# Kernel optimization log

Measured on AMD Instinct MI355X. Metric: run time of the kernel, lower is better.

## Reference

```python
import jax, jax.numpy as jnp
import numpy as np


def setup_inputs() -> dict:
    key = jax.random.key(0)
    k1, k2 = jax.random.split(key)
    inputs = jax.random.normal(k1, (4, 8, 24, 24, 64), dtype=jnp.float32)
    gamma = jax.random.normal(k2, (1,), dtype=jnp.float32)
    return {"inputs": inputs, "gamma": gamma}


def reference(inputs, gamma):
    # inputs: (B, D, H, W, C); flatten spatial dims to N = D*H*W
    B, D, H, W, C = inputs.shape
    N = D * H * W
    q = inputs.reshape(B, N, C)                       # proj_query (B, N, C)
    # energy = Q @ Q^T -> (B, N, N)
    energy = jnp.einsum('bnc,bmc->bnm', q, q)
    attention = jax.nn.softmax(energy, axis=-1)       # softmax over last axis
    out = jnp.einsum('bnm,bmc->bnc', attention, q)    # (B, N, C)
    out = out.reshape(B, D, H, W, C)
    return gamma * out + inputs
```

## Files before the change

kernel.cpp:

```cpp
#include <hip/hip_runtime.h>

typedef __bf16 bf16_t;
typedef bf16_t bf16x8 __attribute__((ext_vector_type(8)));
typedef float  f32x4  __attribute__((ext_vector_type(4)));
typedef unsigned int u32;
typedef u32    u32x4  __attribute__((ext_vector_type(4)));
typedef unsigned short u16;

#define B_SZ   4
#define N_SZ   4608
#define C_SZ   64
#define KVB    32
#define QROWS  32
#define NKVT   (N_SZ / KVB)
#define NQT    (N_SZ / QROWS)
#define WV     4
#define SPLIT  4
#define TPC    (NKVT / SPLIT)
#define TPW    (TPC / WV)
#define NBLK   (B_SZ * NQT * SPLIT)
#define RSC    1.2011224087864498f
#define THR    11.0f

__device__ __forceinline__ f32x4 mfma16(bf16x8 a, bf16x8 b, f32x4 c) {
  return __builtin_amdgcn_mfma_f32_16x16x32_bf16(a, b, c, 0, 0, 0);
}

__device__ __forceinline__ u32 pk2(float a, float b) {
  u16 ua = __builtin_bit_cast(u16, (bf16_t)a);
  u16 ub = __builtin_bit_cast(u16, (bf16_t)b);
  return (u32)ua | ((u32)ub << 16);
}

__global__ __launch_bounds__(256) void transform_k(
    const float* __restrict__ in, bf16_t* __restrict__ khi,
    bf16_t* __restrict__ klo, bf16_t* __restrict__ vt) {
  __shared__ float tile[64 * 65];
  const int bid = blockIdx.x;
  const int b  = bid / 72;
  const int n0 = (bid - b * 72) * 64;
  const int t  = threadIdx.x;
  {
    const int nl = t >> 2, c0 = (t & 3) * 16;
    const float* src = in + ((size_t)(b * N_SZ + n0 + nl)) * C_SZ + c0;
    float v[16];
    *(float4*)(v +  0) = *(const float4*)(src +  0);
    *(float4*)(v +  4) = *(const float4*)(src +  4);
    *(float4*)(v +  8) = *(const float4*)(src +  8);
    *(float4*)(v + 12) = *(const float4*)(src + 12);
    bf16x8 h8[2], l8[2];
#pragma unroll
    for (int i = 0; i < 16; ++i) {
      const float vs = RSC * v[i];
      bf16_t h = (bf16_t)vs;
      h8[i >> 3][i & 7] = h;
      l8[i >> 3][i & 7] = (bf16_t)(vs - (float)h);
      tile[nl * 65 + c0 + i] = v[i];
    }
    bf16_t* dh = khi + ((size_t)(b * N_SZ + n0 + nl)) * C_SZ + c0;
    bf16_t* dl = klo + ((size_t)(b * N_SZ + n0 + nl)) * C_SZ + c0;
    *(bf16x8*)(dh) = h8[0]; *(bf16x8*)(dh + 8) = h8[1];
    *(bf16x8*)(dl) = l8[0]; *(bf16x8*)(dl + 8) = l8[1];
  }
  __syncthreads();
  {
    const int c = t >> 2, m0 = (t & 3) * 16;
    bf16x8 o[2];
#pragma unroll
    for (int i = 0; i < 16; ++i)
      o[i >> 3][i & 7] = (bf16_t)tile[(m0 + i) * 65 + c];
    bf16_t* dst = vt + ((size_t)(b * C_SZ + c)) * N_SZ + n0 + m0;
    *(bf16x8*)(dst) = o[0]; *(bf16x8*)(dst + 8) = o[1];
  }
}

#define LOAD_TILE(KV0, KH, KL, VF)                                             \
  {                                                                            \
    _Pragma("unroll")                                                          \
    for (int ct = 0; ct < 2; ++ct)                                             \
      _Pragma("unroll")                                                        \
      for (int ks = 0; ks < 2; ++ks) {                                         \
        const size_t a = (size_t)((KV0) + ct * 16 + c15) * C_SZ + ks * 32 + g * 8; \
        KH[ct][ks] = *(const bf16x8*)(kh_b + a);                               \
        KL[ct][ks] = *(const bf16x8*)(kl_b + a);                               \
      }                                                                        \
    _Pragma("unroll")                                                          \
    for (int co = 0; co < 4; ++co)                                             \
      VF[co] = *(const bf16x8*)(vt_b + (size_t)(co * 16 + c15) * N_SZ + (KV0) + g * 8); \
  }

__global__ __launch_bounds__(256, 2) void attn_part(
    const bf16_t* __restrict__ khi, const bf16_t* __restrict__ klo,
    const bf16_t* __restrict__ vt, float* __restrict__ wsO,
    float* __restrict__ wsML) {
  __shared__ float obuf[256 * 36];
  __shared__ float mlbuf[4 * 2 * 2 * 16];

  const int bid0 = blockIdx.x;
  const int g8   = (bid0 & 7) * (NBLK / 8) + (bid0 >> 3);
  const int b    = g8 / (NQT * SPLIT);
  const int rem  = g8 - b * (NQT * SPLIT);
  const int s    = rem / NQT;
  const int qt   = rem - s * NQT;
  const int blk  = (b * NQT + qt) * SPLIT + s;
  const int t  = threadIdx.x;
  const int w  = t >> 6, l = t & 63;
  const int c15 = l & 15, g = l >> 4;

  const bf16_t* kh_b = khi + (size_t)b * N_SZ * C_SZ;
  const bf16_t* kl_b = klo + (size_t)b * N_SZ * C_SZ;
  const bf16_t* vt_b = vt  + (size_t)b * C_SZ * N_SZ;

  bf16x8 qh[2][2], ql[2][2];
#pragma unroll
  for (int j = 0; j < 2; ++j)
#pragma unroll
    for (int ks = 0; ks < 2; ++ks) {
      const size_t a = (size_t)(qt * QROWS + j * 16 + c15) * C_SZ + ks * 32 + g * 8;
      qh[j][ks] = *(const bf16x8*)(kh_b + a);
      ql[j][ks] = *(const bf16x8*)(kl_b + a);
    }

  f32x4 acc[4][2];
#pragma unroll
  for (int co = 0; co < 4; ++co)
#pragma unroll
    for (int j = 0; j < 2; ++j)
      acc[co][j] = (f32x4){0.f, 0.f, 0.f, 0.f};
  float m_j[2] = {-3.0e38f, -3.0e38f}, l_j[2] = {0.f, 0.f};

  const int sA = ((l >> 4) & 1) * 32 + c15;
  const int sB = sA + 16;
  const bool hi_half = (l >= 32);

  bf16x8 khf[2][2], klf[2][2], vf[4];
  LOAD_TILE((s * TPC + w) * KVB, khf, klf, vf);

  for (int it = 0; it < TPW; ++it) {
    const int itn = (it + 1 < TPW) ? it + 1 : 0;
    const int kvn = (s * TPC + w + itn * WV) * KVB;
    bf16x8 nkh[2][2], nkl[2][2], nvf[4];
    LOAD_TILE(kvn, nkh, nkl, nvf);

    f32x4 sv[2][2];
#pragma unroll
    for (int j = 0; j < 2; ++j)
#pragma unroll
      for (int ct = 0; ct < 2; ++ct) {
        f32x4 a = (f32x4){0.f, 0.f, 0.f, 0.f};
#pragma unroll
        for (int ks = 0; ks < 2; ++ks) {
          a = mfma16(khf[ct][ks], qh[j][ks], a);
          a = mfma16(khf[ct][ks], ql[j][ks], a);
          a = mfma16(klf[ct][ks], qh[j][ks], a);
        }
        sv[j][ct] = a;
      }

#pragma unroll
    for (int j = 0; j < 2; ++j) {
      float mx = fmaxf(fmaxf(fmaxf(sv[j][0][0], sv[j][0][1]), fmaxf(sv[j][0][2], sv[j][0][3])),
                       fmaxf(fmaxf(sv[j][1][0], sv[j][1][1]), fmaxf(sv[j][1][2], sv[j][1][3])));
      mx = fmaxf(mx, __shfl_xor(mx, 16, 64));
      mx = fmaxf(mx, __shfl_xor(mx, 32, 64));
      if (__any(mx > m_j[j] + THR)) {
        const float mn = fmaxf(m_j[j], mx);
        const float sc = exp2f(m_j[j] - mn);
        m_j[j] = mn;
        l_j[j] *= sc;
#pragma unroll
        for (int co = 0; co < 4; ++co)
          acc[co][j] *= sc;
      }
      float rs = 0.f;
#pragma unroll
      for (int ct = 0; ct < 2; ++ct)
#pragma unroll
        for (int r = 0; r < 4; ++r) {
          const float e = exp2f(sv[j][ct][r] - m_j[j]);
          sv[j][ct][r] = e;
          rs += e;
        }
      rs += __shfl_xor(rs, 16, 64);
      rs += __shfl_xor(rs, 32, 64);
      l_j[j] += rs;

      const u32 L0 = pk2(sv[j][0][0], sv[j][0][1]);
      const u32 H0 = pk2(sv[j][0][2], sv[j][0][3]);
      const u32 L1 = pk2(sv[j][1][0], sv[j][1][1]);
      const u32 H1 = pk2(sv[j][1][2], sv[j][1][3]);
      const u32 aL0 = (u32)__shfl((int)L0, sA, 64);
      const u32 aL1 = (u32)__shfl((int)L1, sA, 64);
      const u32 aH0 = (u32)__shfl((int)H0, sA, 64);
      const u32 aH1 = (u32)__shfl((int)H1, sA, 64);
      const u32 bL0 = (u32)__shfl((int)L0, sB, 64);
      const u32 bL1 = (u32)__shfl((int)L1, sB, 64);
      const u32 bH0 = (u32)__shfl((int)H0, sB, 64);
      const u32 bH1 = (u32)__shfl((int)H1, sB, 64);
      const u32x4 pw = (u32x4){hi_half ? aL1 : aL0,
                               hi_half ? aH1 : aH0,
                               hi_half ? bL1 : bL0,
                               hi_half ? bH1 : bH0};
      const bf16x8 pfv = __builtin_bit_cast(bf16x8, pw);
#pragma unroll
      for (int co = 0; co < 4; ++co)
        acc[co][j] = mfma16(vf[co], pfv, acc[co][j]);
    }

#pragma unroll
    for (int ct = 0; ct < 2; ++ct)
#pragma unroll
      for (int ks = 0; ks < 2; ++ks) {
        khf[ct][ks] = nkh[ct][ks];
        klf[ct][ks] = nkl[ct][ks];
      }
#pragma unroll
    for (int co = 0; co < 4; ++co)
      vf[co] = nvf[co];
  }

  float* ob = obuf + (size_t)(w * 64 + l) * 36;
#pragma unroll
  for (int co = 0; co < 4; ++co)
#pragma unroll
    for (int j = 0; j < 2; ++j)
      *(f32x4*)(ob + (co * 2 + j) * 4) = acc[co][j];
  if (g == 0) {
#pragma unroll
    for (int j = 0; j < 2; ++j) {
      mlbuf[((w * 2 + j) * 2 + 0) * 16 + c15] = m_j[j];
      mlbuf[((w * 2 + j) * 2 + 1) * 16 + c15] = l_j[j];
    }
  }
  __syncthreads();

  float* pO  = wsO  + (size_t)blk * (QROWS * C_SZ);
  float* pML = wsML + (size_t)blk * (QROWS * 2);
#pragma unroll
  for (int j = 0; j < 2; ++j) {
    float mw[4];
#pragma unroll
    for (int wp = 0; wp < 4; ++wp)
      mw[wp] = mlbuf[((wp * 2 + j) * 2 + 0) * 16 + c15];
    const float ms = fmaxf(fmaxf(mw[0], mw[1]), fmaxf(mw[2], mw[3]));
    float ls = 0.f;
    f32x4 mg = (f32x4){0.f, 0.f, 0.f, 0.f};
#pragma unroll
    for (int wp = 0; wp < 4; ++wp) {
      const float cf = exp2f(mw[wp] - ms);
      ls += cf * mlbuf[((wp * 2 + j) * 2 + 1) * 16 + c15];
      const f32x4 pv = *(const f32x4*)(obuf + (size_t)(wp * 64 + l) * 36 + (w * 2 + j) * 4);
      mg += pv * cf;
    }
    const int q  = j * 16 + c15;
    const int cb = w * 16 + g * 4;
    *(f32x4*)&pO[q * C_SZ + cb] = mg;
    if (w == 0 && g == 0) {
      pML[q * 2 + 0] = ms;
      pML[q * 2 + 1] = ls;
    }
  }
}

__global__ __launch_bounds__(256) void combine_k(
    const float* __restrict__ in, const float* __restrict__ gamma_p,
    const float* __restrict__ wsO, const float* __restrict__ wsML,
    float* __restrict__ out) {
  const int bid = blockIdx.x;
  const int b   = bid / NQT;
  const int qt  = bid - b * NQT;
  const int t   = threadIdx.x;
  const int q   = t >> 3;
  const int c0  = (t & 7) * 8;
  const int blk0 = bid * SPLIT;

  float m[SPLIT], lv[SPLIT];
  f32x4 o0[SPLIT], o1[SPLIT];
#pragma unroll
  for (int s = 0; s < SPLIT; ++s) {
    const float* pML = wsML + (size_t)(blk0 + s) * (QROWS * 2);
    m[s]  = pML[q * 2 + 0];
    lv[s] = pML[q * 2 + 1];
    const float* pO = wsO + (size_t)(blk0 + s) * (QROWS * C_SZ) + q * C_SZ + c0;
    o0[s] = *(const f32x4*)(pO);
    o1[s] = *(const f32x4*)(pO + 4);
  }
  const float ms = fmaxf(fmaxf(m[0], m[1]), fmaxf(m[2], m[3]));
  float ls = 0.f;
  f32x4 a0 = (f32x4){0.f, 0.f, 0.f, 0.f};
  f32x4 a1 = (f32x4){0.f, 0.f, 0.f, 0.f};
#pragma unroll
  for (int s = 0; s < SPLIT; ++s) {
    const float cf = exp2f(m[s] - ms);
    ls += cf * lv[s];
    a0 += o0[s] * cf;
    a1 += o1[s] * cf;
  }
  const float sc = gamma_p[0] / ls;
  const int row = qt * QROWS + q;
  const size_t base = ((size_t)(b * N_SZ + row)) * C_SZ + c0;
  const float4 i0 = *(const float4*)(in + base);
  const float4 i1 = *(const float4*)(in + base + 4);
  float4 v0, v1;
  v0.x = a0[0] * sc + i0.x; v0.y = a0[1] * sc + i0.y;
  v0.z = a0[2] * sc + i0.z; v0.w = a0[3] * sc + i0.w;
  v1.x = a1[0] * sc + i1.x; v1.y = a1[1] * sc + i1.y;
  v1.z = a1[2] * sc + i1.z; v1.w = a1[3] * sc + i1.w;
  *(float4*)(out + base)     = v0;
  *(float4*)(out + base + 4) = v1;
}

extern "C" void kernel_launch(void* const* d_in, const int* in_sizes, int n_in,
                              void* d_out, int out_size, void* d_ws, size_t ws_size,
                              hipStream_t stream) {
  const float* in = (const float*)d_in[0];
  const float* gp = (const float*)d_in[1];
  float* op = (float*)d_out;
  const size_t plane = (size_t)B_SZ * N_SZ * C_SZ;
  bf16_t* khi = (bf16_t*)d_ws;
  bf16_t* klo = khi + plane;
  bf16_t* vt  = klo + plane;
  float*  wsO  = (float*)((char*)d_ws + 3 * plane * sizeof(bf16_t));
  float*  wsML = wsO + (size_t)NBLK * (QROWS * C_SZ);

  hipLaunchKernelGGL(transform_k, dim3(288), dim3(256), 0, stream, in, khi, klo, vt);
  hipLaunchKernelGGL(attn_part, dim3(NBLK), dim3(256), 0, stream,
                     khi, klo, vt, wsO, wsML);
  hipLaunchKernelGGL(combine_k, dim3(B_SZ * NQT), dim3(256), 0, stream,
                     in, gp, wsO, wsML, op);
}
```

Before: 187.8 us.

## Switch attention inner loop to 32x32x16 MFMA with permlane32 swap for P

Reworks the split-KV attention kernel to use 32x32x16 bf16 MFMA tiles instead of 16x16x32. Each wave now computes a full 32x32 score tile, and the probability fragment is rearranged with permlane32_swap rather than eight cross-lane shuffles. The exp uses raw v_exp_f32, and the occupancy hint is raised from 2 to 4 blocks per CU. The explicit register double-buffered prefetch of K/V tiles is dropped, which may expose load latency; the higher occupancy is meant to hide it instead.

```diff
diff --git a/kernel.cpp b/kernel.cpp
--- a/kernel.cpp
+++ b/kernel.cpp
@@ -3,8 +3,10 @@
 typedef __bf16 bf16_t;
 typedef bf16_t bf16x8 __attribute__((ext_vector_type(8)));
 typedef float  f32x4  __attribute__((ext_vector_type(4)));
+typedef float  f32x16 __attribute__((ext_vector_type(16)));
 typedef unsigned int u32;
 typedef u32    u32x4  __attribute__((ext_vector_type(4)));
+typedef int    i32x2  __attribute__((ext_vector_type(2)));
 typedef unsigned short u16;
 
 #define B_SZ   4
@@ -22,14 +24,22 @@
 #define RSC    1.2011224087864498f
 #define THR    11.0f
 
-__device__ __forceinline__ f32x4 mfma16(bf16x8 a, bf16x8 b, f32x4 c) {
-  return __builtin_amdgcn_mfma_f32_16x16x32_bf16(a, b, c, 0, 0, 0);
-}
-
+__device__ __forceinline__ f32x16 mfma32(bf16x8 a, bf16x8 b, f32x16 c) {
+  return __builtin_amdgcn_mfma_f32_32x32x16_bf16(a, b, c, 0, 0, 0);
+}
 __device__ __forceinline__ u32 pk2(float a, float b) {
   u16 ua = __builtin_bit_cast(u16, (bf16_t)a);
   u16 ub = __builtin_bit_cast(u16, (bf16_t)b);
   return (u32)ua | ((u32)ub << 16);
+}
+__device__ __forceinline__ float ex2(float x) {
+  float r;
+  asm("v_exp_f32 %0, %1" : "=v"(r) : "v"(x));
+  return r;
+}
+__device__ __forceinline__ void plswap(u32& a, u32& b) {
+  i32x2 r = __builtin_amdgcn_permlane32_swap((int)a, (int)b, false, false);
+  a = (u32)r.x; b = (u32)r.y;
 }
 
 __global__ __launch_bounds__(256) void transform_k(
@@ -74,27 +84,12 @@
   }
 }
 
-#define LOAD_TILE(KV0, KH, KL, VF)                                             \
-  {                                                                            \
-    _Pragma("unroll")                                                          \
-    for (int ct = 0; ct < 2; ++ct)                                             \
-      _Pragma("unroll")                                                        \
-      for (int ks = 0; ks < 2; ++ks) {                                         \
-        const size_t a = (size_t)((KV0) + ct * 16 + c15) * C_SZ + ks * 32 + g * 8; \
-        KH[ct][ks] = *(const bf16x8*)(kh_b + a);                               \
-        KL[ct][ks] = *(const bf16x8*)(kl_b + a);                               \
-      }                                                                        \
-    _Pragma("unroll")                                                          \
-    for (int co = 0; co < 4; ++co)                                             \
-      VF[co] = *(const bf16x8*)(vt_b + (size_t)(co * 16 + c15) * N_SZ + (KV0) + g * 8); \
-  }
-
-__global__ __launch_bounds__(256, 2) void attn_part(
+__global__ __launch_bounds__(256, 4) void attn_part(
     const bf16_t* __restrict__ khi, const bf16_t* __restrict__ klo,
     const bf16_t* __restrict__ vt, float* __restrict__ wsO,
     float* __restrict__ wsML) {
-  __shared__ float obuf[256 * 36];
-  __shared__ float mlbuf[4 * 2 * 2 * 16];
+  __shared__ float obuf[256 * 33];
+  __shared__ float mlbuf[WV][2][32];
 
   const int bid0 = blockIdx.x;
   const int g8   = (bid0 & 7) * (NBLK / 8) + (bid0 >> 3);
@@ -105,159 +100,133 @@
   const int blk  = (b * NQT + qt) * SPLIT + s;
   const int t  = threadIdx.x;
   const int w  = t >> 6, l = t & 63;
-  const int c15 = l & 15, g = l >> 4;
+  const int q31 = l & 31, h = l >> 5;
 
   const bf16_t* kh_b = khi + (size_t)b * N_SZ * C_SZ;
   const bf16_t* kl_b = klo + (size_t)b * N_SZ * C_SZ;
   const bf16_t* vt_b = vt  + (size_t)b * C_SZ * N_SZ;
 
-  bf16x8 qh[2][2], ql[2][2];
-#pragma unroll
-  for (int j = 0; j < 2; ++j)
-#pragma unroll
-    for (int ks = 0; ks < 2; ++ks) {
-      const size_t a = (size_t)(qt * QROWS + j * 16 + c15) * C_SZ + ks * 32 + g * 8;
-      qh[j][ks] = *(const bf16x8*)(kh_b + a);
-      ql[j][ks] = *(const bf16x8*)(kl_b + a);
-    }
-
-  f32x4 acc[4][2];
-#pragma unroll
-  for (int co = 0; co < 4; ++co)
-#pragma unroll
-    for (int j = 0; j < 2; ++j)
-      acc[co][j] = (f32x4){0.f, 0.f, 0.f, 0.f};
-  float m_j[2] = {-3.0e38f, -3.0e38f}, l_j[2] = {0.f, 0.f};
-
-  const int sA = ((l >> 4) & 1) * 32 + c15;
-  const int sB = sA + 16;
-  const bool hi_half = (l >= 32);
-
-  bf16x8 khf[2][2], klf[2][2], vf[4];
-  LOAD_TILE((s * TPC + w) * KVB, khf, klf, vf);
+  bf16x8 qh[4], ql[4];
+  {
+    const bf16_t* qrh = kh_b + (size_t)(qt * QROWS + q31) * C_SZ + 8 * h;
+    const bf16_t* qrl = kl_b + (size_t)(qt * QROWS + q31) * C_SZ + 8 * h;
+#pragma unroll
+    for (int ks = 0; ks < 4; ++ks) {
+      qh[ks] = *(const bf16x8*)(qrh + 16 * ks);
+      ql[ks] = *(const bf16x8*)(qrl + 16 * ks);
+    }
+  }
+
+  f32x16 acc0 = {0,0,0,0,0,0,0,0,0,0,0,0,0,0,0,0};
+  f32x16 acc1 = {0,0,0,0,0,0,0,0,0,0,0,0,0,0,0,0};
+  float m_r = -3.0e38f, l_r = 0.f;
 
   for (int it = 0; it < TPW; ++it) {
-    const int itn = (it + 1 < TPW) ? it + 1 : 0;
-    const int kvn = (s * TPC + w + itn * WV) * KVB;
-    bf16x8 nkh[2][2], nkl[2][2], nvf[4];
-    LOAD_TILE(kvn, nkh, nkl, nvf);
-
-    f32x4 sv[2][2];
-#pragma unroll
-    for (int j = 0; j < 2; ++j)
-#pragma unroll
-      for (int ct = 0; ct < 2; ++ct) {
-        f32x4 a = (f32x4){0.f, 0.f, 0.f, 0.f};
-#pragma unroll
-        for (int ks = 0; ks < 2; ++ks) {
-          a = mfma16(khf[ct][ks], qh[j][ks], a);
-          a = mfma16(khf[ct][ks], ql[j][ks], a);
-          a = mfma16(klf[ct][ks], qh[j][ks], a);
-        }
-        sv[j][ct] = a;
+    const int kv0 = (s * TPC + w + it * WV) * KVB;
+
+    bf16x8 kah[4], kal[4];
+    {
+      const bf16_t* krh = kh_b + (size_t)(kv0 + q31) * C_SZ + 8 * h;
+      const bf16_t* krl = kl_b + (size_t)(kv0 + q31) * C_SZ + 8 * h;
+#pragma unroll
+      for (int ks = 0; ks < 4; ++ks) {
+        kah[ks] = *(const bf16x8*)(krh + 16 * ks);
+        kal[ks] = *(const bf16x8*)(krl + 16 * ks);
       }
-
-#pragma unroll
-    for (int j = 0; j < 2; ++j) {
-      float mx = fmaxf(fmaxf(fmaxf(sv[j][0][0], sv[j][0][1]), fmaxf(sv[j][0][2], sv[j][0][3])),
-                       fmaxf(fmaxf(sv[j][1][0], sv[j][1][1]), fmaxf(sv[j][1][2], sv[j][1][3])));
-      mx = fmaxf(mx, __shfl_xor(mx, 16, 64));
-      mx = fmaxf(mx, __shfl_xor(mx, 32, 64));
-      if (__any(mx > m_j[j] + THR)) {
-        const float mn = fmaxf(m_j[j], mx);
-        const float sc = exp2f(m_j[j] - mn);
-        m_j[j] = mn;
-        l_j[j] *= sc;
-#pragma unroll
-        for (int co = 0; co < 4; ++co)
-          acc[co][j] *= sc;
-      }
-      float rs = 0.f;
-#pragma unroll
-      for (int ct = 0; ct < 2; ++ct)
-#pragma unroll
-        for (int r = 0; r < 4; ++r) {
-          const float e = exp2f(sv[j][ct][r] - m_j[j]);
-          sv[j][ct][r] = e;
-          rs += e;
-        }
-      rs += __shfl_xor(rs, 16, 64);
-      rs += __shfl_xor(rs, 32, 64);
-      l_j[j] += rs;
-
-      const u32 L0 = pk2(sv[j][0][0], sv[j][0][1]);
-      const u32 H0 = pk2(sv[j][0][2], sv[j][0][3]);
-      const u32 L1 = pk2(sv[j][1][0], sv[j][1][1]);
-      const u32 H1 = pk2(sv[j][1][2], sv[j][1][3]);
-      const u32 aL0 = (u32)__shfl((int)L0, sA, 64);
-      const u32 aL1 = (u32)__shfl((int)L1, sA, 64);
-      const u32 aH0 = (u32)__shfl((int)H0, sA, 64);
-      const u32 aH1 = (u32)__shfl((int)H1, sA, 64);
-      const u32 bL0 = (u32)__shfl((int)L0, sB, 64);
-      const u32 bL1 = (u32)__shfl((int)L1, sB, 64);
-      const u32 bH0 = (u32)__shfl((int)H0, sB, 64);
-      const u32 bH1 = (u32)__shfl((int)H1, sB, 64);
-      const u32x4 pw = (u32x4){hi_half ? aL1 : aL0,
-                               hi_half ? aH1 : aH0,
-                               hi_half ? bL1 : bL0,
-                               hi_half ? bH1 : bH0};
-      const bf16x8 pfv = __builtin_bit_cast(bf16x8, pw);
-#pragma unroll
-      for (int co = 0; co < 4; ++co)
-        acc[co][j] = mfma16(vf[co], pfv, acc[co][j]);
-    }
-
-#pragma unroll
-    for (int ct = 0; ct < 2; ++ct)
-#pragma unroll
-      for (int ks = 0; ks < 2; ++ks) {
-        khf[ct][ks] = nkh[ct][ks];
-        klf[ct][ks] = nkl[ct][ks];
-      }
-#pragma unroll
-    for (int co = 0; co < 4; ++co)
-      vf[co] = nvf[co];
-  }
-
-  float* ob = obuf + (size_t)(w * 64 + l) * 36;
-#pragma unroll
-  for (int co = 0; co < 4; ++co)
-#pragma unroll
-    for (int j = 0; j < 2; ++j)
-      *(f32x4*)(ob + (co * 2 + j) * 4) = acc[co][j];
-  if (g == 0) {
-#pragma unroll
-    for (int j = 0; j < 2; ++j) {
-      mlbuf[((w * 2 + j) * 2 + 0) * 16 + c15] = m_j[j];
-      mlbuf[((w * 2 + j) * 2 + 1) * 16 + c15] = l_j[j];
-    }
+    }
+
+    f32x16 sv = {0,0,0,0,0,0,0,0,0,0,0,0,0,0,0,0};
+#pragma unroll
+    for (int ks = 0; ks < 4; ++ks) {
+      sv = mfma32(kah[ks], qh[ks], sv);
+      sv = mfma32(kah[ks], ql[ks], sv);
+      sv = mfma32(kal[ks], qh[ks], sv);
+    }
+
+    bf16x8 va[2][2];
+#pragma unroll
+    for (int cb = 0; cb < 2; ++cb)
+#pragma unroll
+      for (int ki = 0; ki < 2; ++ki)
+        va[cb][ki] = *(const bf16x8*)(vt_b + (size_t)(cb * 32 + q31) * N_SZ
+                                      + kv0 + 16 * ki + 8 * h);
+
+    float mx = sv[0];
+#pragma unroll
+    for (int r = 1; r < 16; ++r) mx = fmaxf(mx, sv[r]);
+    mx = fmaxf(mx, __shfl_xor(mx, 32, 64));
+    if (__any(mx > m_r + THR)) {
+      const float mn = fmaxf(m_r, mx);
+      const float sc = ex2(m_r - mn);
+      m_r = mn;
+      l_r *= sc;
+#pragma unroll
+      for (int r = 0; r < 16; ++r) { acc0[r] *= sc; acc1[r] *= sc; }
+    }
+    float rs = 0.f;
+#pragma unroll
+    for (int r = 0; r < 16; ++r) {
+      const float e = ex2(sv[r] - m_r);
+      sv[r] = e;
+      rs += e;
+    }
+    rs += __shfl_xor(rs, 32, 64);
+    l_r += rs;
+
+    u32 pw[8];
+#pragma unroll
+    for (int wd = 0; wd < 8; ++wd) pw[wd] = pk2(sv[2 * wd], sv[2 * wd + 1]);
+    plswap(pw[0], pw[2]); plswap(pw[1], pw[3]);
+    plswap(pw[4], pw[6]); plswap(pw[5], pw[7]);
+    const bf16x8 pb1 = __builtin_bit_cast(bf16x8, (u32x4){pw[0], pw[1], pw[2], pw[3]});
+    const bf16x8 pb2 = __builtin_bit_cast(bf16x8, (u32x4){pw[4], pw[5], pw[6], pw[7]});
+
+    acc0 = mfma32(va[0][0], pb1, acc0);
+    acc0 = mfma32(va[0][1], pb2, acc0);
+    acc1 = mfma32(va[1][0], pb1, acc1);
+    acc1 = mfma32(va[1][1], pb2, acc1);
+  }
+
+  {
+    float* ob = obuf + (size_t)(w * 64 + l) * 33;
+#pragma unroll
+    for (int r = 0; r < 16; ++r) ob[r] = acc0[r];
+#pragma unroll
+    for (int r = 0; r < 16; ++r) ob[16 + r] = acc1[r];
+    if (l < 32) { mlbuf[w][0][l] = m_r; mlbuf[w][1][l] = l_r; }
   }
   __syncthreads();
 
   float* pO  = wsO  + (size_t)blk * (QROWS * C_SZ);
   float* pML = wsML + (size_t)blk * (QROWS * 2);
-#pragma unroll
-  for (int j = 0; j < 2; ++j) {
-    float mw[4];
-#pragma unroll
-    for (int wp = 0; wp < 4; ++wp)
-      mw[wp] = mlbuf[((wp * 2 + j) * 2 + 0) * 16 + c15];
+  {
+    float mw[4], lw[4];
+#pragma unroll
+    for (int wp = 0; wp < 4; ++wp) {
+      mw[wp] = mlbuf[wp][0][q31];
+      lw[wp] = mlbuf[wp][1][q31];
+    }
     const float ms = fmaxf(fmaxf(mw[0], mw[1]), fmaxf(mw[2], mw[3]));
     float ls = 0.f;
-    f32x4 mg = (f32x4){0.f, 0.f, 0.f, 0.f};
+    f32x4 r0 = (f32x4){0.f, 0.f, 0.f, 0.f};
+    f32x4 r1 = (f32x4){0.f, 0.f, 0.f, 0.f};
+    const int ofs = (w >> 1) * 16 + 8 * (w & 1);
 #pragma unroll
     for (int wp = 0; wp < 4; ++wp) {
-      const float cf = exp2f(mw[wp] - ms);
-      ls += cf * mlbuf[((wp * 2 + j) * 2 + 1) * 16 + c15];
-      const f32x4 pv = *(const f32x4*)(obuf + (size_t)(wp * 64 + l) * 36 + (w * 2 + j) * 4);
-      mg += pv * cf;
-    }
-    const int q  = j * 16 + c15;
-    const int cb = w * 16 + g * 4;
-    *(f32x4*)&pO[q * C_SZ + cb] = mg;
-    if (w == 0 && g == 0) {
-      pML[q * 2 + 0] = ms;
-      pML[q * 2 + 1] = ls;
+      const float cf = ex2(mw[wp] - ms);
+      ls += cf * lw[wp];
+      const float* src = obuf + (size_t)(wp * 64 + l) * 33 + ofs;
+#pragma unroll
+      for (int i = 0; i < 4; ++i) r0[i] += cf * src[i];
+#pragma unroll
+      for (int i = 0; i < 4; ++i) r1[i] += cf * src[4 + i];
+    }
+    const int cb0 = 16 * w + 4 * h;
+    *(f32x4*)&pO[q31 * C_SZ + cb0]     = r0;
+    *(f32x4*)&pO[q31 * C_SZ + cb0 + 8] = r1;
+    if (w == 0 && l < 32) {
+      pML[l * 2 + 0] = ms;
+      pML[l * 2 + 1] = ls;
     }
   }
 }
```

Measured after the change: 190.0 us. About the same (+1.2%).
